# Kernel tuning notes

Measured on AMD Instinct MI355X. Metric: run time of the kernel, lower is better.

## Reference

```python
import jax, jax.numpy as jnp
from jax import lax
import numpy as np

H = 16        # hidden_size == input_size
L = 8         # num_layers


def _lstm_layer(x_seq, Wih, Whh, bih, bhh):
    # x_seq: [B, T, H] -> outputs [B, T, H]; PyTorch gate order i,f,g,o
    B = x_seq.shape[0]
    b = bih + bhh  # [4H]

    def step(carry, xt):
        h, c = carry
        gates = xt @ Wih.T + h @ Whh.T + b  # [B, 4H]
        i, f, g, o = jnp.split(gates, 4, axis=-1)
        c = jax.nn.sigmoid(f) * c + jax.nn.sigmoid(i) * jnp.tanh(g)
        h = jax.nn.sigmoid(o) * jnp.tanh(c)
        return (h, c), h

    h0 = jnp.zeros((B, H), x_seq.dtype)
    (_, _), hs = lax.scan(step, (h0, h0), jnp.swapaxes(x_seq, 0, 1))
    return jnp.swapaxes(hs, 0, 1)  # [B, T, H]


def setup_inputs() -> dict:
    key = jax.random.key(0)
    ks = jax.random.split(key, 9)
    s = 1.0 / np.sqrt(H)  # PyTorch default init scale
    x = jax.random.normal(ks[0], (2048, 512, H), dtype=jnp.float32)
    W_ih = jax.random.uniform(ks[1], (L, 4 * H, H), jnp.float32, -s, s)
    W_hh = jax.random.uniform(ks[2], (L, 4 * H, H), jnp.float32, -s, s)
    b_ih = jax.random.uniform(ks[3], (L, 4 * H), jnp.float32, -s, s)
    b_hh = jax.random.uniform(ks[4], (L, 4 * H), jnp.float32, -s, s)
    Wp = jax.random.uniform(ks[5], (3, H), jnp.float32, -s, s)
    bp = jax.random.uniform(ks[6], (3,), jnp.float32, -s, s)
    Wo = jax.random.uniform(ks[7], (3, H), jnp.float32, -s, s)
    bo = jax.random.uniform(ks[8], (3,), jnp.float32, -s, s)
    return {"x": x, "W_ih": W_ih, "W_hh": W_hh, "b_ih": b_ih, "b_hh": b_hh,
            "Wp": Wp, "bp": bp, "Wo": Wo, "bo": bo}


def reference(x, W_ih, W_hh, b_ih, b_hh, Wp, bp, Wo, bo):
    h = x
    for l in range(L):  # fixed small layer count
        h = _lstm_layer(h, W_ih[l], W_hh[l], b_ih[l], b_hh[l])
    last = h[:, -1, :]                       # [B, H]
    position = last @ Wp.T + bp              # [B, 3]
    orientation = jnp.tanh(last @ Wo.T + bo) # [B, 3]
    return jnp.concatenate((position, orientation), axis=1)  # [B, 6]
```

## Files before the change

### kernel.cpp

```cpp
#include <hip/hip_runtime.h>
#include <math.h>

typedef _Float16 f16x8 __attribute__((ext_vector_type(8)));
typedef _Float16 f16x2 __attribute__((ext_vector_type(2)));
typedef float    f32x4 __attribute__((ext_vector_type(4)));

constexpr int kT    = 512;
constexpr int kH    = 16;
constexpr int kL    = 8;
constexpr int kG    = 64;
constexpr int kNB   = 8;
constexpr int kPad  = 24;
constexpr int kRows = 9;
constexpr int kSlots= 16;
constexpr int kLyr  = kL + 1;
constexpr int kSE   = kLyr * kRows * kPad;
constexpr int kIters= 33;
constexpr int kLastS= kIters * 16 - 1;

constexpr float kL2E = 1.4426950408889634f;

__device__ __forceinline__ float ex2(float w)  { return __builtin_amdgcn_exp2f(w); }
__device__ __forceinline__ float rcp1p(float e){ return __builtin_amdgcn_rcpf(1.0f + e); }
__device__ __forceinline__ void  cbar()        { asm volatile("" ::: "memory"); }

__global__ __launch_bounds__(512, 2)
void lstm_sp(const float* __restrict__ x,
             const float* __restrict__ Wih, const float* __restrict__ Whh,
             const float* __restrict__ bih, const float* __restrict__ bhh,
             const float* __restrict__ Wp,  const float* __restrict__ bpos,
             const float* __restrict__ Wo,  const float* __restrict__ bori,
             float* __restrict__ out)
{
    const int tid  = threadIdx.x;
    const int l    = tid >> 6;
    const int lane = tid & 63;
    const int n    = lane & 15;
    const int q    = lane >> 4;
    const int bn   = n & 7;
    const bool bact = ((q >> 1) == (n >> 3));

    __shared__ __align__(16) _Float16 hb[kSlots][kLyr][kRows][kPad];
    __shared__ int cnt[kL];

    {
        int* hz = (int*)&hb[0][0][0][0];
        for (int i = tid; i < (int)(sizeof(hb) / 4); i += 512) hz[i] = 0;
        if (tid < kL) cnt[tid] = -1;
    }
    __syncthreads();

    const float asc = ((n & 3) == 2) ? (-2.0f * kL2E) : (-kL2E);
    auto loadA = [&](const float* W, int T) -> f16x8 {
        const int wrow = (n & 3) * 16 + (n >> 2) + 4 * (q >> 1) + 8 * T;
        const float* src = W + (size_t)l * kG * kH + wrow * kH;
        f16x8 a;
        #pragma unroll
        for (int j = 0; j < 8; ++j) {
            const int u = (q & 1) * 4 + (j >> 1) + 8 * (j & 1);
            a[j] = (_Float16)(asc * src[u]);
        }
        return a;
    };
    const f16x8 A1T0 = loadA(Wih, 0), A2T0 = loadA(Whh, 0);
    const f16x8 A1T1 = loadA(Wih, 1), A2T1 = loadA(Whh, 1);

    const int u0 = q + 4 * (n >> 3);
    f32x4 bias0, bias1;
    #pragma unroll
    for (int r = 0; r < 4; ++r) {
        const float sc = (r == 2) ? (-2.0f * kL2E) : (-kL2E);
        const int g0 = l * kG + r * 16 + u0;
        bias0[r] = sc * (bih[g0] + bhh[g0]);
        bias1[r] = sc * (bih[g0 + 8] + bhh[g0 + 8]);
    }

    const int boff = (bact ? bn * kPad : 8 * kPad) + (q & 1) * 8;
    const _Float16* b1b = &hb[0][l    ][0][0] + boff;
    const _Float16* b2b = &hb[0][l + 1][0][0] + boff;
    _Float16* hw  = &hb[0][l + 1][bn][2 * u0];
    _Float16* xw  = &hb[0][0][lane >> 3][2 * (lane & 7)];

    const int xa = lane & 7;
    const float* xg_ptr =
        x + ((size_t)(blockIdx.x * kNB + (lane >> 3)) * kT) * kH;
    float xg0 = 0.f, xg1 = 0.f;
    if (l == 0) {
        #pragma unroll
        for (int t = 0; t < 2; ++t) {
            f16x2 xp = { (_Float16)xg_ptr[t * kH + xa],
                         (_Float16)xg_ptr[t * kH + xa + 8] };
            *(f16x2*)(xw + t * kSE) = xp;
        }
        xg0 = xg_ptr[2 * kH + xa];
        xg1 = xg_ptr[2 * kH + xa + 8];
    }

    f16x8 B2r = *(const f16x8*)(b2b);
    {
        const f16x8 B1p = *(const f16x8*)(b1b);
    }
    const f16x8 B1p = *(const f16x8*)(b1b);
    f32x4 dIn0 = __builtin_amdgcn_mfma_f32_16x16x32_f16(A1T0, B1p, bias0, 0, 0, 0);
    f32x4 dIn1 = __builtin_amdgcn_mfma_f32_16x16x32_f16(A1T1, B1p, bias1, 0, 0, 0);

    float c0 = 0.f, c1 = 0.f;

    volatile const int* upc = (l > 0)      ? &cnt[l - 1] : nullptr;
    volatile const int* dnc = (l < kL - 1) ? &cnt[l + 1] : nullptr;

    #pragma unroll 1
    for (int it = 0; it < kIters; ++it) {
        const int sb = it * 16;
        #pragma unroll
        for (int k = 0; k < 16; ++k) {
            const int s = sb + k;

            if ((k & 1) == 0 && l > 0) {
                int need = s + 1; if (need > kLastS) need = kLastS;
                while (*upc < need) __builtin_amdgcn_s_sleep(1);
                cbar();
            }
            if ((k == 0 || k == 8) && l < kL - 1) {
                const int need = (k == 0) ? (sb - 8) : sb;
                while (*dnc < need) __builtin_amdgcn_s_sleep(1);
                cbar();
            }

            const int  slot1  = ((k + 1) & 15) * kSE;
            const int  slot2  = ((k + 2) & 15) * kSE;
            const bool active = ((unsigned)(s - l) < (unsigned)kT);

            const f16x8 B1n = *(const f16x8*)(b1b + slot1);

            f32x4 d0 = __builtin_amdgcn_mfma_f32_16x16x32_f16(A2T0, B2r, dIn0, 0, 0, 0);
            f32x4 d1 = __builtin_amdgcn_mfma_f32_16x16x32_f16(A2T1, B2r, dIn1, 0, 0, 0);

            float h0, h1;
            {
                const float si = rcp1p(ex2(d0[0]));
                const float sf = rcp1p(ex2(d0[1]));
                const float sg = rcp1p(ex2(d0[2]));
                const float so = rcp1p(ex2(d0[3]));
                const float tgp = fmaf(-4.0f * kL2E, sg, 2.0f * kL2E);
                float cn = fmaf(sf, c0, si * tgp);
                cn = active ? cn : 0.0f;
                c0 = cn;
                h0 = so * fmaf(2.0f, rcp1p(ex2(cn)), -1.0f);
            }
            {
                const float si = rcp1p(ex2(d1[0]));
                const float sf = rcp1p(ex2(d1[1]));
                const float sg = rcp1p(ex2(d1[2]));
                const float so = rcp1p(ex2(d1[3]));
                const float tgp = fmaf(-4.0f * kL2E, sg, 2.0f * kL2E);
                float cn = fmaf(sf, c1, si * tgp);
                cn = active ? cn : 0.0f;
                c1 = cn;
                h1 = so * fmaf(2.0f, rcp1p(ex2(cn)), -1.0f);
            }

            f16x2 hp = { (_Float16)h0, (_Float16)h1 };
            *(f16x2*)(hw + slot1) = hp;

            if (l == 0) {
                f16x2 xp = { (_Float16)xg0, (_Float16)xg1 };
                *(f16x2*)(xw + slot2) = xp;
                int tn = s + 3; if (tn > kT - 1) tn = kT - 1;
                xg0 = xg_ptr[(size_t)tn * kH + xa];
                xg1 = xg_ptr[(size_t)tn * kH + xa + 8];
            }

            B2r = *(const f16x8*)(b2b + slot1);

            dIn0 = __builtin_amdgcn_mfma_f32_16x16x32_f16(A1T0, B1n, bias0, 0, 0, 0);
            dIn1 = __builtin_amdgcn_mfma_f32_16x16x32_f16(A1T1, B1n, bias1, 0, 0, 0);

            if (k & 1) {
                cbar();
                if (lane == 0) *(volatile int*)&cnt[l] = s;
            }
        }
    }

    __syncthreads();

    if (l == kL - 1) {
        const int bb = lane >> 3;
        const int r  = lane & 7;
        if (r < 6) {
            const bool  isP   = (r < 3);
            const float* wrow = isP ? (Wp + r * kH) : (Wo + (r - 3) * kH);
            float acc = isP ? bpos[r] : bori[r - 3];
            #pragma unroll
            for (int u = 0; u < kH; ++u) {
                const int p = 2 * (u & 7) + (u >> 3);
                acc = fmaf((float)hb[7][kL][bb][p], wrow[u], acc);
            }
            if (!isP) acc = fmaf(2.0f, rcp1p(ex2(-2.0f * kL2E * acc)), -1.0f);
            out[(size_t)(blockIdx.x * kNB + bb) * 6 + r] = acc;
        }
    }
}

extern "C" void kernel_launch(void* const* d_in, const int* in_sizes, int n_in,
                              void* d_out, int out_size, void* d_ws, size_t ws_size,
                              hipStream_t stream) {
    const float* x    = (const float*)d_in[0];
    const float* Wih  = (const float*)d_in[1];
    const float* Whh  = (const float*)d_in[2];
    const float* bih  = (const float*)d_in[3];
    const float* bhh  = (const float*)d_in[4];
    const float* Wp   = (const float*)d_in[5];
    const float* bpos = (const float*)d_in[6];
    const float* Wo   = (const float*)d_in[7];
    const float* bori = (const float*)d_in[8];
    float* out = (float*)d_out;

    const int B = in_sizes[0] / (kT * kH);
    lstm_sp<<<dim3(B / kNB), dim3(512), 0, stream>>>(x, Wih, Whh, bih, bhh,
                                                     Wp, bpos, Wo, bori, out);
}
```

Baseline: 301.7 us.

## Replace per-layer spin-wait counters with block barriers and bpermute recurrent state

Drops the shared-memory counter handshake between layer wavefronts and uses one workgroup barrier per step, with layer l lagging two steps per layer (2*l skew). The recurrent h operand is now rebuilt in registers through ds_bpermute instead of being read back from LDS, which takes an LDS round trip off the serial critical path. The x prefetch is deepened to keep layer 0 fed. The cost is a full 512-thread barrier every step and a longer pipeline skew, which adds more iterations' worth of latency.

```diff
diff --git a/kernel.cpp b/kernel.cpp
--- a/kernel.cpp
+++ b/kernel.cpp
@@ -16,21 +16,19 @@
 constexpr int kLyr  = kL + 1;
 constexpr int kSE   = kLyr * kRows * kPad;
 constexpr int kIters= 33;
-constexpr int kLastS= kIters * 16 - 1;
 
 constexpr float kL2E = 1.4426950408889634f;
 
 __device__ __forceinline__ float ex2(float w)  { return __builtin_amdgcn_exp2f(w); }
 __device__ __forceinline__ float rcp1p(float e){ return __builtin_amdgcn_rcpf(1.0f + e); }
-__device__ __forceinline__ void  cbar()        { asm volatile("" ::: "memory"); }
 
 __global__ __launch_bounds__(512, 2)
-void lstm_sp(const float* __restrict__ x,
-             const float* __restrict__ Wih, const float* __restrict__ Whh,
-             const float* __restrict__ bih, const float* __restrict__ bhh,
-             const float* __restrict__ Wp,  const float* __restrict__ bpos,
-             const float* __restrict__ Wo,  const float* __restrict__ bori,
-             float* __restrict__ out)
+void lstm_bar(const float* __restrict__ x,
+              const float* __restrict__ Wih, const float* __restrict__ Whh,
+              const float* __restrict__ bih, const float* __restrict__ bhh,
+              const float* __restrict__ Wp,  const float* __restrict__ bpos,
+              const float* __restrict__ Wo,  const float* __restrict__ bori,
+              float* __restrict__ out)
 {
     const int tid  = threadIdx.x;
     const int l    = tid >> 6;
@@ -41,12 +39,10 @@
     const bool bact = ((q >> 1) == (n >> 3));
 
     __shared__ __align__(16) _Float16 hb[kSlots][kLyr][kRows][kPad];
-    __shared__ int cnt[kL];
 
     {
         int* hz = (int*)&hb[0][0][0][0];
         for (int i = tid; i < (int)(sizeof(hb) / 4); i += 512) hz[i] = 0;
-        if (tid < kL) cnt[tid] = -1;
     }
     __syncthreads();
 
@@ -76,62 +72,52 @@
     }
 
     const int boff = (bact ? bn * kPad : 8 * kPad) + (q & 1) * 8;
-    const _Float16* b1b = &hb[0][l    ][0][0] + boff;
-    const _Float16* b2b = &hb[0][l + 1][0][0] + boff;
-    _Float16* hw  = &hb[0][l + 1][bn][2 * u0];
-    _Float16* xw  = &hb[0][0][lane >> 3][2 * (lane & 7)];
+    const _Float16* b1b = &hb[0][l][0][0] + boff;
+    _Float16* hw = &hb[0][l + 1][bn][2 * u0];
+    _Float16* xw = &hb[0][0][lane >> 3][2 * (lane & 7)];
+
+    const int bpbase = 4 * bn + 32 * (q & 1);
+    const int mska   = bact ? -1 : 0;
 
     const int xa = lane & 7;
     const float* xg_ptr =
         x + ((size_t)(blockIdx.x * kNB + (lane >> 3)) * kT) * kH;
-    float xg0 = 0.f, xg1 = 0.f;
+    float xa0 = 0.f, xa1 = 0.f, xb0 = 0.f, xb1 = 0.f;
     if (l == 0) {
         #pragma unroll
-        for (int t = 0; t < 2; ++t) {
+        for (int t = 0; t < 3; ++t) {
             f16x2 xp = { (_Float16)xg_ptr[t * kH + xa],
                          (_Float16)xg_ptr[t * kH + xa + 8] };
-            *(f16x2*)(xw + t * kSE) = xp;
-        }
-        xg0 = xg_ptr[2 * kH + xa];
-        xg1 = xg_ptr[2 * kH + xa + 8];
-    }
-
-    f16x8 B2r = *(const f16x8*)(b2b);
-    {
-        const f16x8 B1p = *(const f16x8*)(b1b);
-    }
-    const f16x8 B1p = *(const f16x8*)(b1b);
+            *(f16x2*)(xw + ((t + 15) & 15) * kSE) = xp;
+        }
+        xa0 = xg_ptr[3 * kH + xa]; xa1 = xg_ptr[3 * kH + xa + 8];
+        xb0 = xg_ptr[4 * kH + xa]; xb1 = xg_ptr[4 * kH + xa + 8];
+    }
+    __syncthreads();
+
+    const f16x8 B1p = *(const f16x8*)(b1b + 15 * kSE);
     f32x4 dIn0 = __builtin_amdgcn_mfma_f32_16x16x32_f16(A1T0, B1p, bias0, 0, 0, 0);
     f32x4 dIn1 = __builtin_amdgcn_mfma_f32_16x16x32_f16(A1T1, B1p, bias1, 0, 0, 0);
 
+    f16x8 B2r;
+    #pragma unroll
+    for (int j = 0; j < 8; ++j) B2r[j] = (_Float16)0.f;
+
     float c0 = 0.f, c1 = 0.f;
-
-    volatile const int* upc = (l > 0)      ? &cnt[l - 1] : nullptr;
-    volatile const int* dnc = (l < kL - 1) ? &cnt[l + 1] : nullptr;
+    const int tl = 2 * l;
 
     #pragma unroll 1
     for (int it = 0; it < kIters; ++it) {
-        const int sb = it * 16;
+        const int wb = it * 16;
         #pragma unroll
         for (int k = 0; k < 16; ++k) {
-            const int s = sb + k;
-
-            if ((k & 1) == 0 && l > 0) {
-                int need = s + 1; if (need > kLastS) need = kLastS;
-                while (*upc < need) __builtin_amdgcn_s_sleep(1);
-                cbar();
-            }
-            if ((k == 0 || k == 8) && l < kL - 1) {
-                const int need = (k == 0) ? (sb - 8) : sb;
-                while (*dnc < need) __builtin_amdgcn_s_sleep(1);
-                cbar();
-            }
-
-            const int  slot1  = ((k + 1) & 15) * kSE;
-            const int  slot2  = ((k + 2) & 15) * kSE;
-            const bool active = ((unsigned)(s - l) < (unsigned)kT);
-
-            const f16x8 B1n = *(const f16x8*)(b1b + slot1);
+            const int w = wb + k;
+            const int slotR = k * kSE;
+            const int slotW = ((k + 1) & 15) * kSE;
+            const int slotX = ((k + 2) & 15) * kSE;
+            const bool active = ((unsigned)(w - tl) < (unsigned)kT);
+
+            const f16x8 B1n = *(const f16x8*)(b1b + slotR);
 
             f32x4 d0 = __builtin_amdgcn_mfma_f32_16x16x32_f16(A2T0, B2r, dIn0, 0, 0, 0);
             f32x4 d1 = __builtin_amdgcn_mfma_f32_16x16x32_f16(A2T1, B2r, dIn1, 0, 0, 0);
@@ -161,25 +147,32 @@
             }
 
             f16x2 hp = { (_Float16)h0, (_Float16)h1 };
-            *(f16x2*)(hw + slot1) = hp;
+            union { f16x2 h; int i; } uh; uh.h = hp;
+            const int hpi = uh.i;
+            const int w0 = __builtin_amdgcn_ds_bpermute(bpbase      , hpi) & mska;
+            const int w1 = __builtin_amdgcn_ds_bpermute(bpbase + 64 , hpi) & mska;
+            const int w2 = __builtin_amdgcn_ds_bpermute(bpbase + 128, hpi) & mska;
+            const int w3 = __builtin_amdgcn_ds_bpermute(bpbase + 192, hpi) & mska;
+
+            *(f16x2*)(hw + slotW) = hp;
+
+            union { int i[4]; f16x8 v; } ub;
+            ub.i[0] = w0; ub.i[1] = w1; ub.i[2] = w2; ub.i[3] = w3;
+            B2r = ub.v;
 
             if (l == 0) {
-                f16x2 xp = { (_Float16)xg0, (_Float16)xg1 };
-                *(f16x2*)(xw + slot2) = xp;
-                int tn = s + 3; if (tn > kT - 1) tn = kT - 1;
-                xg0 = xg_ptr[(size_t)tn * kH + xa];
-                xg1 = xg_ptr[(size_t)tn * kH + xa + 8];
-            }
-
-            B2r = *(const f16x8*)(b2b + slot1);
+                f16x2 xp = { (_Float16)xa0, (_Float16)xa1 };
+                *(f16x2*)(xw + slotX) = xp;
+                xa0 = xb0; xa1 = xb1;
+                int tn = w + 5; if (tn > kT - 1) tn = kT - 1;
+                xb0 = xg_ptr[(size_t)tn * kH + xa];
+                xb1 = xg_ptr[(size_t)tn * kH + xa + 8];
+            }
 
             dIn0 = __builtin_amdgcn_mfma_f32_16x16x32_f16(A1T0, B1n, bias0, 0, 0, 0);
             dIn1 = __builtin_amdgcn_mfma_f32_16x16x32_f16(A1T1, B1n, bias1, 0, 0, 0);
 
-            if (k & 1) {
-                cbar();
-                if (lane == 0) *(volatile int*)&cnt[l] = s;
-            }
+            asm volatile("s_waitcnt lgkmcnt(0)\n\ts_barrier" ::: "memory");
         }
     }
 
@@ -195,7 +188,7 @@
             #pragma unroll
             for (int u = 0; u < kH; ++u) {
                 const int p = 2 * (u & 7) + (u >> 3);
-                acc = fmaf((float)hb[7][kL][bb][p], wrow[u], acc);
+                acc = fmaf((float)hb[14][kL][bb][p], wrow[u], acc);
             }
             if (!isP) acc = fmaf(2.0f, rcp1p(ex2(-2.0f * kL2E * acc)), -1.0f);
             out[(size_t)(blockIdx.x * kNB + bb) * 6 + r] = acc;
@@ -218,6 +211,6 @@
     float* out = (float*)d_out;
 
     const int B = in_sizes[0] / (kT * kH);
-    lstm_sp<<<dim3(B / kNB), dim3(512), 0, stream>>>(x, Wih, Whh, bih, bhh,
-                                                     Wp, bpos, Wo, bori, out);
+    lstm_bar<<<dim3(B / kNB), dim3(512), 0, stream>>>(x, Wih, Whh, bih, bhh,
+                                                      Wp, bpos, Wo, bori, out);
 }
```

Result: no change. 295.9 us (-1.9%).
